# Kernel optimization log

Measured on AMD Instinct MI355X. Metric: run time of the kernel, lower is better.

Reference implementation:

```python
import math
import jax, jax.numpy as jnp
import numpy as np
from jax.scipy.special import xlogy

B, N, INP, E = 128, 16, 1024, 512
MU, CLF, PLCY = 512, 512, 512
M = N - 1          # merges (full tree)
T = N + M          # total tree tokens
L = N + M - 1      # logits matrix side
NOISE_STD, MASK_VAL = 0.01, -9e20
SFTMX_EPS, STD_EPS = 1e-20, 1e-20


def _mlp3(x, w1, b1, w2, b2, w3, b3):
    h = jax.nn.relu(x @ w1 + b1)
    h = jax.nn.relu(h @ w2 + b2)
    return h @ w3 + b3


def _lin(key, fi, fo):
    lim = math.sqrt(6.0 / (fi + fo))  # xavier uniform
    return (jax.random.uniform(key, (fi, fo), minval=-lim, maxval=lim, dtype=jnp.float32),
            jnp.full((fo,), 0.001, dtype=jnp.float32))


def setup_inputs():
    key = jax.random.key(0)
    ks = jax.random.split(key, 16)
    inp = {"x": jax.random.normal(ks[0], (B, N, INP), dtype=jnp.float32)}
    inp["lift_w"], inp["lift_b"] = _lin(ks[1], INP, E)
    inp["unlift_w"], inp["unlift_b"] = _lin(ks[2], E, INP)
    inp["enc_w1"], inp["enc_b1"] = _lin(ks[3], 2 * E, MU)
    inp["enc_w2"], inp["enc_b2"] = _lin(ks[4], MU, MU)
    inp["enc_w3"], inp["enc_b3"] = _lin(ks[5], MU, E)
    inp["dec_w1"], inp["dec_b1"] = _lin(ks[6], E, MU)
    inp["dec_w2"], inp["dec_b2"] = _lin(ks[7], MU, MU)
    inp["dec_w3"], inp["dec_b3"] = _lin(ks[8], MU, 2 * E)
    inp["clf_w1"], inp["clf_b1"] = _lin(ks[9], E, CLF)
    inp["clf_w2"], inp["clf_b2"] = _lin(ks[10], CLF, CLF)
    inp["clf_w3"], inp["clf_b3"] = _lin(ks[11], CLF, 2)
    inp["pol_w1"], inp["pol_b1"] = _lin(ks[12], 2 * E, PLCY)
    inp["pol_w2"], inp["pol_b2"] = _lin(ks[13], PLCY, PLCY)
    inp["pol_w3"], inp["pol_b3"] = _lin(ks[14], PLCY, 1)
    return inp


def _forward(x, lift_w, lift_b, unlift_w, unlift_b,
             enc_w1, enc_b1, enc_w2, enc_b2, enc_w3, enc_b3,
             dec_w1, dec_b1, dec_w2, dec_b2, dec_w3, dec_b3,
             clf_w1, clf_b1, clf_w2, clf_b2, clf_w3, clf_b3,
             pol_w1, pol_b1, pol_w2, pol_b2, pol_w3, pol_b3):
    sg = jax.lax.stop_gradient
    enc = lambda z: _mlp3(z, enc_w1, enc_b1, enc_w2, enc_b2, enc_w3, enc_b3)
    dec = lambda z: _mlp3(z, dec_w1, dec_b1, dec_w2, dec_b2, dec_w3, dec_b3)
    clf = lambda z: _mlp3(z, clf_w1, clf_b1, clf_w2, clf_b2, clf_w3, clf_b3)
    pol = lambda z: _mlp3(z, pol_w1, pol_b1, pol_w2, pol_b2, pol_w3, pol_b3)
    base = jax.random.key(42)
    b_idx = jnp.arange(B)

    # lift + noise
    u = x @ lift_w + lift_b
    u = u + NOISE_STD * jax.random.normal(jax.random.fold_in(base, 7), u.shape, u.dtype)

    logits_mtx = jnp.full((B, L, L), MASK_VAL, dtype=jnp.float32)
    # iter 0: score all ordered pairs (i,j), i != j, among input tokens (vectorized)
    ii, jj = np.where(~np.eye(N, dtype=bool))                 # P = N*(N-1) static pairs
    pair_x = jnp.concatenate([u[:, ii], u[:, jj]], axis=-1)   # [B,P,2E]
    logits_mtx = logits_mtx.at[:, ii, jj].set(pol(sg(pair_x))[..., 0])

    active = jnp.tile(jnp.arange(N, dtype=jnp.int32), (B, 1))
    step_losses = jnp.zeros(B, dtype=jnp.float32)
    entropies = jnp.zeros(B, dtype=jnp.float32)
    actions, log_probs, rewards = [], [], []

    for it in range(M):
        A = active.shape[1]  # = N - it (active-token count at entry)
        if it > 0:
            nt = N + it - 1                      # newest merged token (last in active)
            act = active[:, :-1]                 # [B, A-1] older active tokens
            u_act = u[b_idx[:, None], act]       # [B, A-1, E]
            u_nt = jnp.broadcast_to(u[:, nt][:, None, :], u_act.shape)
            lg_f = pol(sg(jnp.concatenate([u_nt, u_act], -1)))[..., 0]
            lg_b = pol(sg(jnp.concatenate([u_act, u_nt], -1)))[..., 0]
            logits_mtx = logits_mtx.at[b_idx[:, None], nt, act].set(lg_f)
            logits_mtx = logits_mtx.at[b_idx[:, None], act, nt].set(lg_b)

        flat = logits_mtx.reshape(B, L * L)      # temp == 1 for learned policy
        p = jax.nn.softmax(flat, axis=1)
        P2 = L * L
        p_adj = (p + SFTMX_EPS) / (1.0 + P2 * SFTMX_EPS)
        val_norm = SFTMX_EPS / (1.0 + P2 * SFTMX_EPS)
        opt_norm = A * (A - 1)
        nopt = P2 - opt_norm
        entrop = -(jnp.sum(xlogy(p_adj, p_adj), axis=1)
                   - nopt * (val_norm * math.log(val_norm))) / math.log(opt_norm)
        entropies = entropies + entrop

        # multinomial sample over flattened (masked) logits matrix
        sflat = jax.random.categorical(jax.random.fold_in(base, 100 + it), flat)
        s0, s1 = sflat // L, sflat % L
        sample = jnp.stack([s0, s1], axis=1)     # [B,2]
        actions.append(sample)
        log_probs.append(jnp.log(p[b_idx, sflat]))

        # mask out rows/cols of the merged tokens
        logits_mtx = logits_mtx.at[b_idx[:, None], sample, :].set(MASK_VAL)
        logits_mtx = logits_mtx.at[b_idx[:, None], :, sample].set(MASK_VAL)

        # remove the two sampled tokens from the active set (order-preserving)
        keep = (active != s0[:, None].astype(active.dtype)) & (active != s1[:, None].astype(active.dtype))
        order = jnp.argsort((~keep).astype(jnp.int32), axis=1, stable=True)
        active = jnp.take_along_axis(active, order[:, :A - 2], axis=1)

        pair = jnp.concatenate([u[b_idx, s0], u[b_idx, s1]], axis=1)  # [B,2E]
        true_s = sg(pair)
        pred_s = dec(enc(true_s))
        osl = jnp.sum((pred_s - true_s) ** 2, axis=1) / (2 * E)
        step_losses = step_losses + osl
        rewards.append(-sg(osl))

        # merge: encode pair (grad flows into u here) + noise, append to tree
        mg = enc(pair)
        mg = mg + NOISE_STD * jax.random.normal(jax.random.fold_in(base, 1000 + it), mg.shape, mg.dtype)
        u = jnp.concatenate([u, mg[:, None, :]], axis=1)
        active = jnp.concatenate([active, jnp.full((B, 1), N + it, dtype=active.dtype)], axis=1)

    actions = jnp.stack(actions, axis=1)    # [B,M,2]
    log_probs = jnp.stack(log_probs, axis=1)
    rewards = jnp.stack(rewards, axis=1)

    # top-down decode
    d = jnp.zeros_like(u)
    d = d.at[b_idx[:, None], active].set(u[b_idx[:, None], active])  # seed remaining active (root)
    clf_rows = []
    for it in range(M):
        tok = T - 1 - it
        mgd = d[:, tok]
        unmg = dec(mgd).reshape(B, 2, E)
        d = d.at[b_idx[:, None], actions[:, M - 1 - it]].set(unmg)
        clf_rows.append(clf(sg(mgd)))
    clf_pred = jnp.concatenate(
        [jnp.stack(clf_rows, axis=1), clf(sg(d[:, :N]))[:, ::-1, :]], axis=1)  # [B,M+N,2]
    clf_lbl = jnp.tile(jnp.concatenate(
        [jnp.ones(M, dtype=jnp.int32), jnp.zeros(N, dtype=jnp.int32)]), (B, 1))

    step_losses = step_losses / M
    entropies = entropies / M
    mvg = rewards.reshape(-1)  # B*M <= mvg_adv_sz, so moving buffer == current rewards
    rew_n = (rewards - mvg.mean()) / (jnp.std(mvg, ddof=1) + STD_EPS)
    reinf = jnp.sum(log_probs * rew_n, axis=1)
    recon = d[:, :N] @ unlift_w + unlift_b
    return recon, u, d, step_losses, entropies, clf_pred, clf_lbl, reinf


def reference(x, lift_w, lift_b, unlift_w, unlift_b,
              enc_w1, enc_b1, enc_w2, enc_b2, enc_w3, enc_b3,
              dec_w1, dec_b1, dec_w2, dec_b2, dec_w3, dec_b3,
              clf_w1, clf_b1, clf_w2, clf_b2, clf_w3, clf_b3,
              pol_w1, pol_b1, pol_w2, pol_b2, pol_w3, pol_b3):
    return _forward(x, lift_w, lift_b, unlift_w, unlift_b,
                    enc_w1, enc_b1, enc_w2, enc_b2, enc_w3, enc_b3,
                    dec_w1, dec_b1, dec_w2, dec_b2, dec_w3, dec_b3,
                    clf_w1, clf_b1, clf_w2, clf_b2, clf_w3, clf_b3,
                    pol_w1, pol_b1, pol_w2, pol_b2, pol_w3, pol_b3)
```

## Files before the change

kernel.cpp:

```cpp
#include <hip/hip_runtime.h>
#include <cstdint>
#include <cmath>

#define MASKV -9.0e20f

__host__ __device__ inline void tf2x32(uint32_t k0, uint32_t k1, uint32_t& x0, uint32_t& x1){
  uint32_t ks2 = k0 ^ k1 ^ 0x1BD11BDAu;
  x0 += k0; x1 += k1;
#define TFR(r) { x0 += x1; x1 = (x1<<(r))|(x1>>(32-(r))); x1 ^= x0; }
  TFR(13) TFR(15) TFR(26) TFR(6)
  x0 += k1;  x1 += ks2 + 1u;
  TFR(17) TFR(29) TFR(16) TFR(24)
  x0 += ks2; x1 += k0 + 2u;
  TFR(13) TFR(15) TFR(26) TFR(6)
  x0 += k0;  x1 += k1 + 3u;
  TFR(17) TFR(29) TFR(16) TFR(24)
  x0 += k1;  x1 += ks2 + 4u;
  TFR(13) TFR(15) TFR(26) TFR(6)
  x0 += ks2; x1 += k0 + 5u;
#undef TFR
}

__device__ inline uint32_t rbits32(uint32_t k0, uint32_t k1, uint32_t idx){
  uint32_t x0 = 0u, x1 = idx;
  tf2x32(k0, k1, x0, x1);
  return x0 ^ x1;
}

__device__ inline float u01_from_bits(uint32_t bits){
  union { uint32_t u; float f; } c;
  c.u = (bits >> 9) | 0x3f800000u;
  return c.f - 1.0f;
}

__device__ inline float erfinv_f(float x){
  float w = -log1pf(-x*x);
  float p;
  if (w < 5.0f){
    w -= 2.5f;
    p = 2.81022636e-08f;
    p = fmaf(p, w, 3.43273939e-07f);
    p = fmaf(p, w, -3.5233877e-06f);
    p = fmaf(p, w, -4.39150654e-06f);
    p = fmaf(p, w, 0.00021858087f);
    p = fmaf(p, w, -0.00125372503f);
    p = fmaf(p, w, -0.00417768164f);
    p = fmaf(p, w, 0.246640727f);
    p = fmaf(p, w, 1.50140941f);
  } else {
    w = sqrtf(w) - 3.0f;
    p = -0.000200214257f;
    p = fmaf(p, w, 0.000100950558f);
    p = fmaf(p, w, 0.00134934322f);
    p = fmaf(p, w, -0.00367342844f);
    p = fmaf(p, w, 0.00573950773f);
    p = fmaf(p, w, -0.0076224613f);
    p = fmaf(p, w, 0.00943887047f);
    p = fmaf(p, w, 1.00167406f);
    p = fmaf(p, w, 2.83297682f);
  }
  return p * x;
}

__device__ inline float jax_normal(uint32_t k0, uint32_t k1, uint32_t idx){
  float f = u01_from_bits(rbits32(k0, k1, idx));
  float v = fmaf(f, 2.0f, -0.99999994f);
  v = fmaxf(v, -0.99999994f);
  return 1.41421356f * erfinv_f(v);
}

__device__ inline float jax_gumbel(uint32_t k0, uint32_t k1, uint32_t idx){
  float f = u01_from_bits(rbits32(k0, k1, idx));
  f = f + 1.17549435e-38f;
  f = fmaxf(f, 1.17549435e-38f);
  return -logf(-logf(f));
}

template<int ACT>
__global__ __launch_bounds__(256) void gemm_k(
    const float* __restrict__ A, int lda,
    const long* __restrict__ atab, int anblk,
    const float* __restrict__ W, const float* __restrict__ bias,
    float* __restrict__ C, int K, int N,
    long c_base, int c_rdiv, long c_ostride, long c_istride)
{
  __shared__ float As[16][64];
  __shared__ float Ws[16][64];
  int tid = threadIdx.x;
  int c0 = blockIdx.x * 64;
  int r0 = blockIdx.y * 64;
  int lr = tid >> 2;
  int lk = (tid & 3) << 2;
  int wk = tid >> 4;
  int wc = (tid & 15) << 2;
  int tx = tid & 15;
  int ty = tid >> 4;
  long aoff0 = 0, aoff1 = 0;
  if (atab){
    const long* t = atab + (long)(r0 + lr) * anblk;
    aoff0 = t[0];
    if (anblk == 2) aoff1 = t[1];
  } else {
    aoff0 = (long)(r0 + lr) * lda;
  }
  float acc[4][4];
#pragma unroll
  for (int i = 0; i < 4; i++)
#pragma unroll
    for (int j = 0; j < 4; j++) acc[i][j] = 0.f;

  for (int k0 = 0; k0 < K; k0 += 16){
    int ka = k0 + lk;
    long ab = (atab && anblk == 2 && ka >= 512) ? (aoff1 + (ka - 512)) : (aoff0 + ka);
    float4 av = *(const float4*)(A + ab);
    As[lk + 0][lr] = av.x;
    As[lk + 1][lr] = av.y;
    As[lk + 2][lr] = av.z;
    As[lk + 3][lr] = av.w;
    float4 wv = *(const float4*)(W + (long)(k0 + wk) * N + (c0 + wc));
    *(float4*)&Ws[wk][wc] = wv;
    __syncthreads();
#pragma unroll
    for (int kk = 0; kk < 16; kk++){
      float4 a4 = *(const float4*)&As[kk][ty << 2];
      float4 w4 = *(const float4*)&Ws[kk][tx << 2];
      float aa[4] = {a4.x, a4.y, a4.z, a4.w};
      float ww[4] = {w4.x, w4.y, w4.z, w4.w};
#pragma unroll
      for (int i = 0; i < 4; i++)
#pragma unroll
        for (int j = 0; j < 4; j++)
          acc[i][j] = fmaf(aa[i], ww[j], acc[i][j]);
    }
    __syncthreads();
  }
  float4 bv = *(const float4*)(bias + c0 + (tx << 2));
  float bb[4] = {bv.x, bv.y, bv.z, bv.w};
#pragma unroll
  for (int i = 0; i < 4; i++){
    int r = r0 + (ty << 2) + i;
    long off = c_base + (long)(r / c_rdiv) * c_ostride + (long)(r % c_rdiv) * c_istride
               + c0 + (tx << 2);
    float4 v;
    float o0 = acc[i][0] + bb[0], o1 = acc[i][1] + bb[1];
    float o2 = acc[i][2] + bb[2], o3 = acc[i][3] + bb[3];
    if (ACT){ o0 = fmaxf(o0, 0.f); o1 = fmaxf(o1, 0.f); o2 = fmaxf(o2, 0.f); o3 = fmaxf(o3, 0.f); }
    v.x = o0; v.y = o1; v.z = o2; v.w = o3;
    *(float4*)(C + off) = v;
  }
}

__global__ __launch_bounds__(512, 7) void gemm128f_k(
    const float* __restrict__ Y,
    const long* __restrict__ atab,
    const float* __restrict__ b1,
    const float* __restrict__ W2, const float* __restrict__ b2,
    const float* __restrict__ w3,
    const int* __restrict__ scat, float* __restrict__ logits)
{
  __shared__ float As[16][132];
  __shared__ float Ws[16][132];
  int tid = threadIdx.x;
  int c0 = blockIdx.x * 128;
  int r0 = blockIdx.y * 128;
  int tx = tid & 15, ty = tid >> 4;
  int rA = tid >> 2;
  int kq = (tid & 3) << 2;
  long a0r = atab[(long)(r0 + rA) * 2];
  long a1r = atab[(long)(r0 + rA) * 2 + 1];
  int wk = tid >> 5;
  int wc = (tid & 31) << 2;
  float acc[4][8];
#pragma unroll
  for (int i = 0; i < 4; i++)
#pragma unroll
    for (int j = 0; j < 8; j++) acc[i][j] = 0.f;

  for (int k0 = 0; k0 < 512; k0 += 16){
    int ka = k0 + kq;
    float4 p = *(const float4*)(Y + a0r + ka);
    float4 q = *(const float4*)(Y + a1r + ka);
    float4 bb = *(const float4*)(b1 + ka);
    As[kq + 0][rA] = fmaxf(p.x + q.x + bb.x, 0.f);
    As[kq + 1][rA] = fmaxf(p.y + q.y + bb.y, 0.f);
    As[kq + 2][rA] = fmaxf(p.z + q.z + bb.z, 0.f);
    As[kq + 3][rA] = fmaxf(p.w + q.w + bb.w, 0.f);
    *(float4*)&Ws[wk][wc] = *(const float4*)(W2 + (long)(k0 + wk) * 512 + (c0 + wc));
    __syncthreads();
#pragma unroll
    for (int kk = 0; kk < 16; kk++){
      float a4[4], w8[8];
      *(float4*)&a4[0] = *(const float4*)&As[kk][ty << 2];
      *(float4*)&w8[0] = *(const float4*)&Ws[kk][tx << 2];
      *(float4*)&w8[4] = *(const float4*)&Ws[kk][(tx << 2) + 64];
#pragma unroll
      for (int i = 0; i < 4; i++)
#pragma unroll
        for (int j = 0; j < 8; j++)
          acc[i][j] = fmaf(a4[i], w8[j], acc[i][j]);
    }
    __syncthreads();
  }
  float bb[8], w3v[8];
  *(float4*)&bb[0]  = *(const float4*)(b2 + c0 + (tx << 2));
  *(float4*)&bb[4]  = *(const float4*)(b2 + c0 + (tx << 2) + 64);
  *(float4*)&w3v[0] = *(const float4*)(w3 + c0 + (tx << 2));
  *(float4*)&w3v[4] = *(const float4*)(w3 + c0 + (tx << 2) + 64);
#pragma unroll
  for (int i = 0; i < 4; i++){
    float p = 0.f;
#pragma unroll
    for (int j = 0; j < 8; j++)
      p = fmaf(fmaxf(acc[i][j] + bb[j], 0.f), w3v[j], p);
    for (int m = 1; m < 16; m <<= 1) p += __shfl_xor(p, m);
    if (tx == 0){
      int rr = (ty << 2) + i;
      atomicAdd(logits + scat[r0 + rr], p);
    }
  }
}

__global__ __launch_bounds__(256) void gemm64f_k(
    const float* __restrict__ Y,
    const long* __restrict__ atab,
    const float* __restrict__ b1,
    const float* __restrict__ W2, const float* __restrict__ b2,
    const float* __restrict__ w3,
    const int* __restrict__ scat, float* __restrict__ logits)
{
  __shared__ float As[16][64];
  __shared__ float Ws[16][64];
  int tid = threadIdx.x;
  int c0 = blockIdx.x * 64;
  int r0 = blockIdx.y * 64;
  int lr = tid >> 2;
  int lk = (tid & 3) << 2;
  int wk = tid >> 4;
  int wc = (tid & 15) << 2;
  int tx = tid & 15;
  int ty = tid >> 4;
  long a0 = atab[(long)(r0 + lr) * 2];
  long a1 = atab[(long)(r0 + lr) * 2 + 1];
  float acc[4][4];
#pragma unroll
  for (int i = 0; i < 4; i++)
#pragma unroll
    for (int j = 0; j < 4; j++) acc[i][j] = 0.f;

  for (int k0 = 0; k0 < 512; k0 += 16){
    int ka = k0 + lk;
    float4 p = *(const float4*)(Y + a0 + ka);
    float4 q = *(const float4*)(Y + a1 + ka);
    float4 bb = *(const float4*)(b1 + ka);
    As[lk + 0][lr] = fmaxf(p.x + q.x + bb.x, 0.f);
    As[lk + 1][lr] = fmaxf(p.y + q.y + bb.y, 0.f);
    As[lk + 2][lr] = fmaxf(p.z + q.z + bb.z, 0.f);
    As[lk + 3][lr] = fmaxf(p.w + q.w + bb.w, 0.f);
    *(float4*)&Ws[wk][wc] = *(const float4*)(W2 + (long)(k0 + wk) * 512 + (c0 + wc));
    __syncthreads();
#pragma unroll
    for (int kk = 0; kk < 16; kk++){
      float4 a4 = *(const float4*)&As[kk][ty << 2];
      float4 w4 = *(const float4*)&Ws[kk][tx << 2];
      float aa[4] = {a4.x, a4.y, a4.z, a4.w};
      float ww[4] = {w4.x, w4.y, w4.z, w4.w};
#pragma unroll
      for (int i = 0; i < 4; i++)
#pragma unroll
        for (int j = 0; j < 4; j++)
          acc[i][j] = fmaf(aa[i], ww[j], acc[i][j]);
    }
    __syncthreads();
  }
  float bb4[4], w34[4];
  *(float4*)&bb4[0] = *(const float4*)(b2 + c0 + (tx << 2));
  *(float4*)&w34[0] = *(const float4*)(w3 + c0 + (tx << 2));
#pragma unroll
  for (int i = 0; i < 4; i++){
    float p = 0.f;
#pragma unroll
    for (int j = 0; j < 4; j++)
      p = fmaf(fmaxf(acc[i][j] + bb4[j], 0.f), w34[j], p);
    for (int m = 1; m < 16; m <<= 1) p += __shfl_xor(p, m);
    if (tx == 0){
      int r = r0 + (ty << 2) + i;
      atomicAdd(logits + scat[r], p);
    }
  }
}

__global__ __launch_bounds__(256) void rowdot2_k(
    const float* __restrict__ A, int lda,
    const float* __restrict__ W, const float* __restrict__ bias,
    int K, float* __restrict__ out, const int* __restrict__ scat)
{
  int wid = threadIdx.x >> 6, lane = threadIdx.x & 63;
  int r = blockIdx.x * 4 + wid;
  const float* a = A + (long)r * lda;
  float s0 = 0.f, s1 = 0.f;
  for (int k = lane; k < K; k += 64){
    float x = a[k];
    s0 = fmaf(x, W[k * 2], s0);
    s1 = fmaf(x, W[k * 2 + 1], s1);
  }
  for (int off = 32; off > 0; off >>= 1){
    s0 += __shfl_down(s0, off);
    s1 += __shfl_down(s1, off);
  }
  if (lane == 0){
    long o = scat[r];
    out[o] = s0 + bias[0];
    out[o + 1] = s1 + bias[1];
  }
}

__global__ __launch_bounds__(256) void pairmv_k(
    const float* __restrict__ u, const long* __restrict__ tab_pair,
    const float* __restrict__ W, const float* __restrict__ bias,
    float* __restrict__ dst)
{
  __shared__ float s[1024];
  int b = blockIdx.y, tid = threadIdx.x;
  int c = blockIdx.x * 256 + tid;
  long t0 = tab_pair[b * 2], t1 = tab_pair[b * 2 + 1];
  s[tid]       = u[t0 + tid];
  s[tid + 256] = u[t0 + tid + 256];
  s[tid + 512] = u[t1 + tid];
  s[tid + 768] = u[t1 + tid + 256];
  __syncthreads();
  float a0 = 0.f, a1 = 0.f, a2 = 0.f, a3 = 0.f;
#pragma unroll 8
  for (int k = 0; k < 1024; k += 4){
    a0 = fmaf(s[k],     W[(long)k * 512 + c],       a0);
    a1 = fmaf(s[k + 1], W[(long)(k + 1) * 512 + c], a1);
    a2 = fmaf(s[k + 2], W[(long)(k + 2) * 512 + c], a2);
    a3 = fmaf(s[k + 3], W[(long)(k + 3) * 512 + c], a3);
  }
  float v = ((a0 + a1) + (a2 + a3)) + bias[c];
  dst[(long)b * 512 + c] = fmaxf(v, 0.f);
}

__global__ __launch_bounds__(256) void mvrelu_k(
    const float* __restrict__ src, long sstride,
    const float* __restrict__ W, const float* __restrict__ bias,
    float* __restrict__ dst)
{
  __shared__ float s[512];
  int b = blockIdx.y, tid = threadIdx.x;
  int c = blockIdx.x * 256 + tid;
  const float* sr = src + (long)b * sstride;
  s[tid] = sr[tid];
  s[tid + 256] = sr[tid + 256];
  __syncthreads();
  float a0 = 0.f, a1 = 0.f, a2 = 0.f, a3 = 0.f;
#pragma unroll 8
  for (int k = 0; k < 512; k += 4){
    a0 = fmaf(s[k],     W[(long)k * 512 + c],       a0);
    a1 = fmaf(s[k + 1], W[(long)(k + 1) * 512 + c], a1);
    a2 = fmaf(s[k + 2], W[(long)(k + 2) * 512 + c], a2);
    a3 = fmaf(s[k + 3], W[(long)(k + 3) * 512 + c], a3);
  }
  float v = ((a0 + a1) + (a2 + a3)) + bias[c];
  dst[(long)b * 512 + c] = fmaxf(v, 0.f);
}

__global__ __launch_bounds__(256) void lay3z_k(
    const float* __restrict__ src,
    const float* __restrict__ W, const float* __restrict__ bias,
    float* __restrict__ z_all, float* __restrict__ u,
    int it, uint32_t k0, uint32_t k1)
{
  __shared__ float s[512];
  int b = blockIdx.y, tid = threadIdx.x;
  int c = blockIdx.x * 256 + tid;
  const float* sr = src + (long)b * 512;
  s[tid] = sr[tid];
  s[tid + 256] = sr[tid + 256];
  __syncthreads();
  float a0 = 0.f, a1 = 0.f, a2 = 0.f, a3 = 0.f;
#pragma unroll 8
  for (int k = 0; k < 512; k += 4){
    a0 = fmaf(s[k],     W[(long)k * 512 + c],       a0);
    a1 = fmaf(s[k + 1], W[(long)(k + 1) * 512 + c], a1);
    a2 = fmaf(s[k + 2], W[(long)(k + 2) * 512 + c], a2);
    a3 = fmaf(s[k + 3], W[(long)(k + 3) * 512 + c], a3);
  }
  float v = ((a0 + a1) + (a2 + a3)) + bias[c];
  z_all[(long)it * 65536 + (long)b * 512 + c] = v;
  float nv = jax_normal(k0, k1, (uint32_t)(b * 512 + c));
  u[((long)(b * 31 + 16 + it)) * 512 + c] = v + 0.01f * nv;
}

__global__ __launch_bounds__(256) void yrow_k(
    const float* __restrict__ u, const float* __restrict__ W1cat,
    float* __restrict__ Y, int it)
{
  __shared__ float s[512];
  int b = blockIdx.y, tid = threadIdx.x;
  int c = blockIdx.x * 256 + tid;
  const float* sr = u + ((long)(b * 31 + 16 + it)) * 512;
  s[tid] = sr[tid];
  s[tid + 256] = sr[tid + 256];
  __syncthreads();
  float a0 = 0.f, a1 = 0.f, a2 = 0.f, a3 = 0.f;
#pragma unroll 8
  for (int k = 0; k < 512; k += 4){
    a0 = fmaf(s[k],     W1cat[(long)k * 1024 + c],       a0);
    a1 = fmaf(s[k + 1], W1cat[(long)(k + 1) * 1024 + c], a1);
    a2 = fmaf(s[k + 2], W1cat[(long)(k + 2) * 1024 + c], a2);
    a3 = fmaf(s[k + 3], W1cat[(long)(k + 3) * 1024 + c], a3);
  }
  Y[((long)(b * 31 + 16 + it)) * 1024 + c] = (a0 + a1) + (a2 + a3);
}

__global__ __launch_bounds__(256) void rev3_k(
    const float* __restrict__ src,
    const float* __restrict__ W, const float* __restrict__ bias,
    float* __restrict__ dmat, const int* __restrict__ actions, int it)
{
  __shared__ float s[512];
  int b = blockIdx.y, tid = threadIdx.x;
  int p = blockIdx.x * 256 + tid;
  const float* sr = src + (long)b * 512;
  s[tid] = sr[tid];
  s[tid + 256] = sr[tid + 256];
  __syncthreads();
  float a0 = 0.f, a1 = 0.f, a2 = 0.f, a3 = 0.f;
#pragma unroll 8
  for (int k = 0; k < 512; k += 4){
    a0 = fmaf(s[k],     W[(long)k * 1024 + p],       a0);
    a1 = fmaf(s[k + 1], W[(long)(k + 1) * 1024 + p], a1);
    a2 = fmaf(s[k + 2], W[(long)(k + 2) * 1024 + p], a2);
    a3 = fmaf(s[k + 3], W[(long)(k + 3) * 1024 + p], a3);
  }
  float v = ((a0 + a1) + (a2 + a3)) + bias[p];
  int fit = 14 - it;
  int s0 = actions[(b * 15 + fit) * 2];
  int s1 = actions[(b * 15 + fit) * 2 + 1];
  int node = (p < 512) ? s0 : s1;
  int ee = p & 511;
  dmat[((long)(b * 31 + node)) * 512 + ee] = v;
}

__global__ __launch_bounds__(256) void oslb_k(
    const float* __restrict__ pred, const float* __restrict__ u,
    const int* __restrict__ actions, float* __restrict__ sl, float* __restrict__ rew)
{
  int r = blockIdx.x, tid = threadIdx.x;
  int it = r >> 7, b = r & 127;
  int s0 = actions[(b * 15 + it) * 2];
  int s1 = actions[(b * 15 + it) * 2 + 1];
  const float* t0 = u + ((long)(b * 31 + s0)) * 512;
  const float* t1 = u + ((long)(b * 31 + s1)) * 512;
  const float* p = pred + (long)r * 1024;
  float s = 0.f;
  for (int k = tid; k < 512; k += 256){
    float d0 = p[k] - t0[k];       s = fmaf(d0, d0, s);
    float d1 = p[k + 512] - t1[k]; s = fmaf(d1, d1, s);
  }
  __shared__ float red[256];
  red[tid] = s; __syncthreads();
  for (int st = 128; st > 0; st >>= 1){ if (tid < st) red[tid] += red[tid + st]; __syncthreads(); }
  if (tid == 0){
    float osl = red[0] / 1024.0f;
    atomicAdd(sl + b, osl);
    rew[b * 15 + it] = -osl;
  }
}

__global__ __launch_bounds__(256) void init_k(float* __restrict__ lbl,
    float* __restrict__ logits, float* __restrict__ sl, float* __restrict__ ent,
    int* __restrict__ active, float* __restrict__ zb,
    float* __restrict__ W1cat, const float* __restrict__ pol_w1, const float* __restrict__ pol_b3,
    long* __restrict__ tab_init, int* __restrict__ scat_init, long* __restrict__ tab_tok16,
    long* __restrict__ tab_mgd, int* __restrict__ scat_clf, long clf_off)
{
  long i = (long)blockIdx.x * 256 + threadIdx.x;
  if (i < 524288L){
    int k = (int)(i >> 10), n = (int)(i & 1023);
    W1cat[i] = (n < 512) ? pol_w1[(long)k * 512 + n] : pol_w1[(long)(k + 512) * 512 + (n - 512)];
  }
  if (i < 115200L){
    int rem = (int)(i % 900);
    int rr = rem / 30, cc = rem % 30;
    logits[i] = (rr < 16 && cc < 16 && rr != cc) ? pol_b3[0] : MASKV;
  }
  if (i < 30720L){
    int r = (int)i;
    int pk = r >> 7, b = r & 127;
    int ii2 = pk / 15, jr = pk % 15;
    int jj2 = jr + (jr >= ii2 ? 1 : 0);
    tab_init[r * 2]     = ((long)(b * 31 + ii2)) * 1024;
    tab_init[r * 2 + 1] = ((long)(b * 31 + jj2)) * 1024 + 512;
    scat_init[r] = b * 900 + ii2 * 30 + jj2;
  }
  if (i < 3968L){
    lbl[i] = ((i % 31) < 15) ? 1.0f : 0.0f;
    int r = (int)i;
    if (r < 1920){
      scat_clf[r] = (int)(clf_off + (long)(r & 127) * 62 + (r >> 7) * 2);
    } else {
      int rr = r - 1920;
      scat_clf[r] = (int)(clf_off + (long)(rr >> 4) * 62 + 60 - ((rr & 15) << 1));
    }
  }
  if (i < 2048L){
    active[i] = (int)(i & 15);
    tab_tok16[i] = ((long)((i >> 4) * 31 + (i & 15))) * 512;
  }
  if (i < 1920L){
    int it = (int)(i >> 7), b = (int)(i & 127);
    tab_mgd[i] = ((long)(b * 31 + 30 - it)) * 512;
  }
  if (i < 1024L)  zb[i] = 0.f;
  if (i < 128L){ sl[i] = 0.f; ent[i] = 0.f; }
}

__global__ __launch_bounds__(256) void noise_u_k(float* __restrict__ u, uint32_t k0, uint32_t k1){
  uint32_t e = blockIdx.x * 256u + threadIdx.x;
  uint32_t b = e >> 13, rem = e & 8191u, n = rem >> 9, ee = rem & 511u;
  float nr = jax_normal(k0, k1, e);
  long off = ((long)(b * 31u + n)) * 512 + ee;
  u[off] += 0.01f * nr;
}

__global__ __launch_bounds__(256) void build_d_k(float* __restrict__ dmat, const float* __restrict__ u){
  int e = blockIdx.x * 256 + threadIdx.x;
  int b = e >> 9, ee = e & 511;
  long off = ((long)(b * 31 + 30)) * 512 + ee;
  dmat[off] = u[off];
}

__global__ __launch_bounds__(256) void sample_k(float* __restrict__ logits, int* __restrict__ active,
    int* __restrict__ actions, float* __restrict__ lp, float* __restrict__ ent,
    int it, int A, uint32_t k0, uint32_t k1, float log_opt,
    long* __restrict__ tab_loop, int* __restrict__ scat_loop, long* __restrict__ tab_pair,
    const float* __restrict__ pol_b3)
{
  int b = blockIdx.x, tid = threadIdx.x;
  int lane = tid & 63, wid = tid >> 6;
  float* Lg = logits + (long)b * 900;
  __shared__ float rmax[4], rS[4], rT[4], rG[4];
  __shared__ int rGi[4];
  __shared__ int ss0, ss1;

  float v = -3.4e38f;
  for (int j = tid; j < 900; j += 256) v = fmaxf(v, Lg[j]);
#pragma unroll
  for (int m = 32; m; m >>= 1) v = fmaxf(v, __shfl_xor(v, m));
  if (lane == 0) rmax[wid] = v;
  __syncthreads();
  float mx = fmaxf(fmaxf(rmax[0], rmax[1]), fmaxf(rmax[2], rmax[3]));

  float s = 0.f, t = 0.f;
  for (int j = tid; j < 900; j += 256){
    float l = Lg[j];
    float d = l - mx;
    float e = expf(d);
    s += e;
    if (l > MASKV) t = fmaf(e, d, t);
  }
#pragma unroll
  for (int m = 32; m; m >>= 1){ s += __shfl_xor(s, m); t += __shfl_xor(t, m); }
  if (lane == 0){ rS[wid] = s; rT[wid] = t; }

  float bv = -3.4e38f; int bi = 0;
  for (int j = tid; j < 900; j += 256){
    float g = jax_gumbel(k0, k1, (uint32_t)(b * 900 + j));
    float val = Lg[j] + g;
    if (val > bv){ bv = val; bi = j; }
  }
#pragma unroll
  for (int m = 32; m; m >>= 1){
    float ov = __shfl_xor(bv, m); int oi = __shfl_xor(bi, m);
    if (ov > bv || (ov == bv && oi < bi)){ bv = ov; bi = oi; }
  }
  if (lane == 0){ rG[wid] = bv; rGi[wid] = bi; }
  __syncthreads();

  if (tid == 0){
    float S = (rS[0] + rS[1]) + (rS[2] + rS[3]);
    float T = (rT[0] + rT[1]) + (rT[2] + rT[3]);
    ent[b] += -(T / S - logf(S)) / log_opt;
    float gb = rG[0]; int gi = rGi[0];
    for (int w = 1; w < 4; w++){
      if (rG[w] > gb || (rG[w] == gb && rGi[w] < gi)){ gb = rG[w]; gi = rGi[w]; }
    }
    int sf = gi;
    int s0 = sf / 30, s1 = sf % 30;
    ss0 = s0; ss1 = s1;
    actions[(b * 15 + it) * 2] = s0;
    actions[(b * 15 + it) * 2 + 1] = s1;
    lp[b * 15 + it] = Lg[sf] - mx - logf(S);
    tab_pair[b * 2]     = ((long)(b * 31 + s0)) * 512;
    tab_pair[b * 2 + 1] = ((long)(b * 31 + s1)) * 512;
  }
  __syncthreads();
  int s0 = ss0, s1 = ss1;
  if (tid < 30){
    Lg[s0 * 30 + tid] = MASKV;
    Lg[s1 * 30 + tid] = MASKV;
    Lg[tid * 30 + s0] = MASKV;
    Lg[tid * 30 + s1] = MASKV;
  }
  if (tid == 0){
    float b3v = pol_b3[0];
    int buf[16]; int c = 0;
    for (int k = 0; k < A; k++){
      int a = active[b * 16 + k];
      if (a != s0 && a != s1) buf[c++] = a;
    }
    int nt2 = 16 + it;
    buf[c++] = nt2;
    for (int k = 0; k < c; k++) active[b * 16 + k] = buf[k];
    int na2 = c - 1;
    for (int j = 0; j < na2; j++){
      int q = buf[j];
      int r1 = j * 128 + b;
      tab_loop[r1 * 2]     = ((long)(b * 31 + nt2)) * 1024;
      tab_loop[r1 * 2 + 1] = ((long)(b * 31 + q)) * 1024 + 512;
      int sc1 = b * 900 + nt2 * 30 + q;
      scat_loop[r1] = sc1;
      logits[sc1] = b3v;
      int r2 = (na2 + j) * 128 + b;
      tab_loop[r2 * 2]     = ((long)(b * 31 + q)) * 1024;
      tab_loop[r2 * 2 + 1] = ((long)(b * 31 + nt2)) * 1024 + 512;
      int sc2 = b * 900 + q * 30 + nt2;
      scat_loop[r2] = sc2;
      logits[sc2] = b3v;
    }
  }
}

__global__ __launch_bounds__(256) void finalize_k(const float* __restrict__ rew,
    const float* __restrict__ lp, const float* __restrict__ sl, const float* __restrict__ ent,
    float* __restrict__ out_sl, float* __restrict__ out_ent, float* __restrict__ out_reinf)
{
  __shared__ float red[256];
  int tid = threadIdx.x;
  float s = 0.f;
  for (int i = tid; i < 1920; i += 256) s += rew[i];
  red[tid] = s; __syncthreads();
  for (int st = 128; st > 0; st >>= 1){ if (tid < st) red[tid] += red[tid + st]; __syncthreads(); }
  float mean = red[0] / 1920.0f; __syncthreads();
  float v = 0.f;
  for (int i = tid; i < 1920; i += 256){ float x = rew[i] - mean; v = fmaf(x, x, v); }
  red[tid] = v; __syncthreads();
  for (int st = 128; st > 0; st >>= 1){ if (tid < st) red[tid] += red[tid + st]; __syncthreads(); }
  float denom = sqrtf(red[0] / 1919.0f) + 1e-20f;
  if (tid < 128){
    out_sl[tid] = sl[tid] / 15.0f;
    out_ent[tid] = ent[tid] / 15.0f;
    float r = 0.f;
    for (int k = 0; k < 15; k++){
      float rn = (rew[tid * 15 + k] - mean) / denom;
      r = fmaf(lp[tid * 15 + k], rn, r);
    }
    out_reinf[tid] = r;
  }
}

extern "C" void kernel_launch(void* const* d_in, const int* in_sizes, int n_in,
                              void* d_out, int out_size, void* d_ws, size_t ws_size,
                              hipStream_t stream)
{
  const float* x        = (const float*)d_in[0];
  const float* lift_w   = (const float*)d_in[1];
  const float* lift_b   = (const float*)d_in[2];
  const float* unlift_w = (const float*)d_in[3];
  const float* unlift_b = (const float*)d_in[4];
  const float* enc_w1   = (const float*)d_in[5];
  const float* enc_b1   = (const float*)d_in[6];
  const float* enc_w2   = (const float*)d_in[7];
  const float* enc_b2   = (const float*)d_in[8];
  const float* enc_w3   = (const float*)d_in[9];
  const float* enc_b3   = (const float*)d_in[10];
  const float* dec_w1   = (const float*)d_in[11];
  const float* dec_b1   = (const float*)d_in[12];
  const float* dec_w2   = (const float*)d_in[13];
  const float* dec_b2   = (const float*)d_in[14];
  const float* dec_w3   = (const float*)d_in[15];
  const float* dec_b3   = (const float*)d_in[16];
  const float* clf_w1   = (const float*)d_in[17];
  const float* clf_b1   = (const float*)d_in[18];
  const float* clf_w2   = (const float*)d_in[19];
  const float* clf_b2   = (const float*)d_in[20];
  const float* clf_w3   = (const float*)d_in[21];
  const float* clf_b3   = (const float*)d_in[22];
  const float* pol_w1   = (const float*)d_in[23];
  const float* pol_b1   = (const float*)d_in[24];
  const float* pol_w2   = (const float*)d_in[25];
  const float* pol_b2   = (const float*)d_in[26];
  const float* pol_w3   = (const float*)d_in[27];
  const float* pol_b3   = (const float*)d_in[28];

  float* out = (float*)d_out;
  const long U_OFF     = 2097152;
  const long D_OFF     = 4128768;
  const long SL_OFF    = 6160384;
  const long ENT_OFF   = 6160512;
  const long CLF_OFF   = 6160640;
  const long LBL_OFF   = 6168576;
  const long REINF_OFF = 6172544;
  float* recon = out;
  float* u     = out + U_OFF;
  float* dmat  = out + D_OFF;

  char* wsb = (char*)d_ws;
  size_t wo = 0;
  auto alloc = [&](size_t bytes) -> void* {
    void* p = (void*)(wsb + wo);
    wo = (wo + bytes + 255) & ~(size_t)255;
    return p;
  };
  float* logits    = (float*)alloc(115200 * 4);
  float* Y         = (float*)alloc((size_t)3968 * 1024 * 4);
  float* h1clf     = Y;
  float* pbuf      = Y + 2031616;
  float* h2clf     = Y + 2031616;
  float* W1cat     = (float*)alloc((size_t)524288 * 4);
  float* zb        = (float*)alloc(1024 * 4);
  float* h1        = (float*)alloc((size_t)2048 * 512 * 4);
  float* h2        = (float*)alloc((size_t)2048 * 512 * 4);
  float* z_all     = (float*)alloc((size_t)15 * 65536 * 4);
  float* sl        = (float*)alloc(128 * 4);
  float* ent       = (float*)alloc(128 * 4);
  float* lp        = (float*)alloc(1920 * 4);
  float* rew       = (float*)alloc(1920 * 4);
  int*   active    = (int*)alloc(2048 * 4);
  int*   actions   = (int*)alloc(3840 * 4);
  long*  tab_init  = (long*)alloc((size_t)30720 * 2 * 8);
  int*   scat_init = (int*)alloc(30720 * 4);
  long*  tab_loop  = (long*)alloc((size_t)3584 * 2 * 8);
  int*   scat_loop = (int*)alloc(3584 * 4);
  long*  tab_pair  = (long*)alloc(256 * 8);
  long*  tab_mgd   = (long*)alloc(1920 * 8);
  long*  tab_tok16 = (long*)alloc(2048 * 8);
  int*   scat_clf  = (int*)alloc(3968 * 4);
  long*  tab_clf   = tab_mgd;
  (void)ws_size; (void)in_sizes; (void)n_in; (void)out_size;

  uint32_t k7a, k7b, ck0[15], ck1[15], mk0[15], mk1[15];
  { uint32_t a = 0, b = 7; tf2x32(0u, 42u, a, b); k7a = a; k7b = b; }
  for (int it = 0; it < 15; it++){
    { uint32_t a = 0, b = (uint32_t)(100 + it); tf2x32(0u, 42u, a, b); ck0[it] = a; ck1[it] = b; }
    { uint32_t a = 0, b = (uint32_t)(1000 + it); tf2x32(0u, 42u, a, b); mk0[it] = a; mk1[it] = b; }
  }

  auto gemm = [&](int act, const float* A, int lda, const long* atab, int anblk,
                  const float* W, const float* bs, float* C, int rows, int K, int Nn,
                  long cb, int crd, long cos, long cis){
    dim3 g(Nn / 64, rows / 64);
    if (act) gemm_k<1><<<g, 256, 0, stream>>>(A, lda, atab, anblk, W, bs, C, K, Nn, cb, crd, cos, cis);
    else     gemm_k<0><<<g, 256, 0, stream>>>(A, lda, atab, anblk, W, bs, C, K, Nn, cb, crd, cos, cis);
  };

  init_k<<<2048, 256, 0, stream>>>(out + LBL_OFF, logits, sl, ent, active, zb,
                                   W1cat, pol_w1, pol_b3, tab_init, scat_init, tab_tok16,
                                   tab_mgd, scat_clf, CLF_OFF);

  gemm(0, x, 1024, nullptr, 0, lift_w, lift_b, u, 2048, 1024, 512, 0, 16, 15872, 512);
  noise_u_k<<<4096, 256, 0, stream>>>(u, k7a, k7b);

  gemm(0, u, 0, tab_tok16, 1, W1cat, zb, Y, 2048, 512, 1024, 0, 16, 31744, 1024);

  { dim3 g(4, 240);
    gemm128f_k<<<g, 512, 0, stream>>>(Y, tab_init, pol_b1, pol_w2, pol_b2, pol_w3,
                                      scat_init, logits); }

  for (int it = 0; it < 15; it++){
    int A = 16 - it;
    if (it > 0){
      int rows = 256 * (15 - it);
      dim3 g(8, rows / 64);
      gemm64f_k<<<g, 256, 0, stream>>>(Y, tab_loop, pol_b1, pol_w2, pol_b2, pol_w3,
                                       scat_loop, logits);
    }
    float log_opt = (float)log((double)(A * (A - 1)));
    sample_k<<<128, 256, 0, stream>>>(logits, active, actions, lp, ent, it, A,
                                      ck0[it], ck1[it], log_opt,
                                      tab_loop, scat_loop, tab_pair, pol_b3);
    { dim3 g(2, 128);
      pairmv_k<<<g, 256, 0, stream>>>(u, tab_pair, enc_w1, enc_b1, h1); }
    { dim3 g(2, 128);
      mvrelu_k<<<g, 256, 0, stream>>>(h1, 512, enc_w2, enc_b2, h2); }
    { dim3 g(2, 128);
      lay3z_k<<<g, 256, 0, stream>>>(h2, enc_w3, enc_b3, z_all, u, it, mk0[it], mk1[it]); }
    if (it < 14){
      dim3 g(4, 128);
      yrow_k<<<g, 256, 0, stream>>>(u, W1cat, Y, it);
    }
  }

  gemm(1, z_all, 512, nullptr, 0, dec_w1, dec_b1, h1, 1920, 512, 512, 0, 1, 512, 0);
  gemm(1, h1, 512, nullptr, 0, dec_w2, dec_b2, h2, 1920, 512, 512, 0, 1, 512, 0);
  gemm(0, h2, 512, nullptr, 0, dec_w3, dec_b3, pbuf, 1920, 512, 1024, 0, 1, 1024, 0);
  oslb_k<<<1920, 256, 0, stream>>>(pbuf, u, actions, sl, rew);

  build_d_k<<<256, 256, 0, stream>>>(dmat, u);

  for (int it = 0; it < 15; it++){
    int tok = 30 - it;
    { dim3 g(2, 128);
      mvrelu_k<<<g, 256, 0, stream>>>(dmat + (long)tok * 512, 15872, dec_w1, dec_b1, h1); }
    { dim3 g(2, 128);
      mvrelu_k<<<g, 256, 0, stream>>>(h1, 512, dec_w2, dec_b2, h2); }
    { dim3 g(4, 128);
      rev3_k<<<g, 256, 0, stream>>>(h2, dec_w3, dec_b3, dmat, actions, it); }
  }

  gemm(1, dmat, 0, tab_clf, 1, clf_w1, clf_b1, h1clf, 3968, 512, 512, 0, 1, 512, 0);
  gemm(1, h1clf, 512, nullptr, 0, clf_w2, clf_b2, h2clf, 3968, 512, 512, 0, 1, 512, 0);
  rowdot2_k<<<992, 256, 0, stream>>>(h2clf, 512, clf_w3, clf_b3, 512, out, scat_clf);

  gemm(0, dmat, 0, tab_tok16, 1, unlift_w, unlift_b, recon, 2048, 512, 1024,
       0, 16, 16384, 1024);

  finalize_k<<<1, 256, 0, stream>>>(rew, lp, sl, ent,
                                    out + SL_OFF, out + ENT_OFF, out + REINF_OFF);
}
```

Baseline: 2.568 ms.

## Batch four rows per block in sequential matvec kernels and enlarge policy GEMM tile

The per-step matrix-vector kernels in the encoder and decoder loops now handle four batch rows per block, so each weight element loaded from global memory feeds four rows instead of one. This cuts weight traffic per step fourfold but launches a quarter as many blocks. The initial fused policy GEMM now uses a 256-row tile with an 8x8 register tile per thread and a lower occupancy hint, giving more reuse per block at the cost of fewer blocks and more register pressure.

```diff
diff --git a/kernel.cpp b/kernel.cpp
--- a/kernel.cpp
+++ b/kernel.cpp
@@ -150,7 +150,7 @@
   }
 }
 
-__global__ __launch_bounds__(512, 7) void gemm128f_k(
+__global__ __launch_bounds__(512, 4) void gemm128f_k(
     const float* __restrict__ Y,
     const long* __restrict__ atab,
     const float* __restrict__ b1,
@@ -158,46 +158,53 @@
     const float* __restrict__ w3,
     const int* __restrict__ scat, float* __restrict__ logits)
 {
-  __shared__ float As[16][132];
+  __shared__ float As[16][260];
   __shared__ float Ws[16][132];
   int tid = threadIdx.x;
   int c0 = blockIdx.x * 128;
-  int r0 = blockIdx.y * 128;
+  int r0 = blockIdx.y * 256;
   int tx = tid & 15, ty = tid >> 4;
-  int rA = tid >> 2;
-  int kq = (tid & 3) << 2;
+  int rA = tid >> 1;
+  int kh = (tid & 1) << 3;
   long a0r = atab[(long)(r0 + rA) * 2];
   long a1r = atab[(long)(r0 + rA) * 2 + 1];
   int wk = tid >> 5;
   int wc = (tid & 31) << 2;
-  float acc[4][8];
-#pragma unroll
-  for (int i = 0; i < 4; i++)
+  float acc[8][8];
+#pragma unroll
+  for (int i = 0; i < 8; i++)
 #pragma unroll
     for (int j = 0; j < 8; j++) acc[i][j] = 0.f;
 
   for (int k0 = 0; k0 < 512; k0 += 16){
-    int ka = k0 + kq;
-    float4 p = *(const float4*)(Y + a0r + ka);
-    float4 q = *(const float4*)(Y + a1r + ka);
-    float4 bb = *(const float4*)(b1 + ka);
-    As[kq + 0][rA] = fmaxf(p.x + q.x + bb.x, 0.f);
-    As[kq + 1][rA] = fmaxf(p.y + q.y + bb.y, 0.f);
-    As[kq + 2][rA] = fmaxf(p.z + q.z + bb.z, 0.f);
-    As[kq + 3][rA] = fmaxf(p.w + q.w + bb.w, 0.f);
+    float4 p0 = *(const float4*)(Y + a0r + k0 + kh);
+    float4 p1 = *(const float4*)(Y + a0r + k0 + kh + 4);
+    float4 q0 = *(const float4*)(Y + a1r + k0 + kh);
+    float4 q1 = *(const float4*)(Y + a1r + k0 + kh + 4);
+    float4 bv0 = *(const float4*)(b1 + k0 + kh);
+    float4 bv1 = *(const float4*)(b1 + k0 + kh + 4);
+    As[kh + 0][rA] = fmaxf(p0.x + q0.x + bv0.x, 0.f);
+    As[kh + 1][rA] = fmaxf(p0.y + q0.y + bv0.y, 0.f);
+    As[kh + 2][rA] = fmaxf(p0.z + q0.z + bv0.z, 0.f);
+    As[kh + 3][rA] = fmaxf(p0.w + q0.w + bv0.w, 0.f);
+    As[kh + 4][rA] = fmaxf(p1.x + q1.x + bv1.x, 0.f);
+    As[kh + 5][rA] = fmaxf(p1.y + q1.y + bv1.y, 0.f);
+    As[kh + 6][rA] = fmaxf(p1.z + q1.z + bv1.z, 0.f);
+    As[kh + 7][rA] = fmaxf(p1.w + q1.w + bv1.w, 0.f);
     *(float4*)&Ws[wk][wc] = *(const float4*)(W2 + (long)(k0 + wk) * 512 + (c0 + wc));
     __syncthreads();
 #pragma unroll
     for (int kk = 0; kk < 16; kk++){
-      float a4[4], w8[8];
-      *(float4*)&a4[0] = *(const float4*)&As[kk][ty << 2];
+      float a8[8], w8[8];
+      *(float4*)&a8[0] = *(const float4*)&As[kk][ty << 3];
+      *(float4*)&a8[4] = *(const float4*)&As[kk][(ty << 3) + 4];
       *(float4*)&w8[0] = *(const float4*)&Ws[kk][tx << 2];
       *(float4*)&w8[4] = *(const float4*)&Ws[kk][(tx << 2) + 64];
 #pragma unroll
-      for (int i = 0; i < 4; i++)
+      for (int i = 0; i < 8; i++)
 #pragma unroll
         for (int j = 0; j < 8; j++)
-          acc[i][j] = fmaf(a4[i], w8[j], acc[i][j]);
+          acc[i][j] = fmaf(a8[i], w8[j], acc[i][j]);
     }
     __syncthreads();
   }
@@ -207,14 +214,14 @@
   *(float4*)&w3v[0] = *(const float4*)(w3 + c0 + (tx << 2));
   *(float4*)&w3v[4] = *(const float4*)(w3 + c0 + (tx << 2) + 64);
 #pragma unroll
-  for (int i = 0; i < 4; i++){
+  for (int i = 0; i < 8; i++){
     float p = 0.f;
 #pragma unroll
     for (int j = 0; j < 8; j++)
       p = fmaf(fmaxf(acc[i][j] + bb[j], 0.f), w3v[j], p);
     for (int m = 1; m < 16; m <<= 1) p += __shfl_xor(p, m);
     if (tx == 0){
-      int rr = (ty << 2) + i;
+      int rr = (ty << 3) + i;
       atomicAdd(logits + scat[r0 + rr], p);
     }
   }
@@ -314,132 +321,171 @@
   }
 }
 
-__global__ __launch_bounds__(256) void pairmv_k(
-    const float* __restrict__ u, const long* __restrict__ tab_pair,
+template<int ACT>
+__global__ __launch_bounds__(256) void bmv4_k(
+    const float* __restrict__ src, long sbase, long sstride,
+    const long* __restrict__ tab,
     const float* __restrict__ W, const float* __restrict__ bias,
-    float* __restrict__ dst)
-{
-  __shared__ float s[1024];
-  int b = blockIdx.y, tid = threadIdx.x;
+    int K, int N, float* __restrict__ dst, long dbase, long dstride)
+{
+  __shared__ float s[4][1024];
+  int tid = threadIdx.x;
+  int lane = tid & 63, wid = tid >> 6;
+  int b0 = blockIdx.y * 4;
   int c = blockIdx.x * 256 + tid;
-  long t0 = tab_pair[b * 2], t1 = tab_pair[b * 2 + 1];
-  s[tid]       = u[t0 + tid];
-  s[tid + 256] = u[t0 + tid + 256];
-  s[tid + 512] = u[t1 + tid];
-  s[tid + 768] = u[t1 + tid + 256];
+  if (tab){
+    long t0 = tab[(long)(b0 + wid) * 2];
+    long t1 = tab[(long)(b0 + wid) * 2 + 1];
+    if (lane < 32){
+      int k0 = lane << 4;
+      *(float4*)&s[wid][k0]      = *(const float4*)(src + t0 + k0);
+      *(float4*)&s[wid][k0 + 4]  = *(const float4*)(src + t0 + k0 + 4);
+      *(float4*)&s[wid][k0 + 8]  = *(const float4*)(src + t0 + k0 + 8);
+      *(float4*)&s[wid][k0 + 12] = *(const float4*)(src + t0 + k0 + 12);
+    } else {
+      int k0 = (lane - 32) << 4;
+      *(float4*)&s[wid][512 + k0]      = *(const float4*)(src + t1 + k0);
+      *(float4*)&s[wid][512 + k0 + 4]  = *(const float4*)(src + t1 + k0 + 4);
+      *(float4*)&s[wid][512 + k0 + 8]  = *(const float4*)(src + t1 + k0 + 8);
+      *(float4*)&s[wid][512 + k0 + 12] = *(const float4*)(src + t1 + k0 + 12);
+    }
+  } else {
+    const float* sr = src + sbase + (long)(b0 + wid) * sstride;
+    int k0 = lane << 3;
+    *(float4*)&s[wid][k0]     = *(const float4*)(sr + k0);
+    *(float4*)&s[wid][k0 + 4] = *(const float4*)(sr + k0 + 4);
+  }
   __syncthreads();
-  float a0 = 0.f, a1 = 0.f, a2 = 0.f, a3 = 0.f;
-#pragma unroll 8
-  for (int k = 0; k < 1024; k += 4){
-    a0 = fmaf(s[k],     W[(long)k * 512 + c],       a0);
-    a1 = fmaf(s[k + 1], W[(long)(k + 1) * 512 + c], a1);
-    a2 = fmaf(s[k + 2], W[(long)(k + 2) * 512 + c], a2);
-    a3 = fmaf(s[k + 3], W[(long)(k + 3) * 512 + c], a3);
-  }
-  float v = ((a0 + a1) + (a2 + a3)) + bias[c];
-  dst[(long)b * 512 + c] = fmaxf(v, 0.f);
-}
-
-__global__ __launch_bounds__(256) void mvrelu_k(
-    const float* __restrict__ src, long sstride,
-    const float* __restrict__ W, const float* __restrict__ bias,
-    float* __restrict__ dst)
-{
-  __shared__ float s[512];
-  int b = blockIdx.y, tid = threadIdx.x;
-  int c = blockIdx.x * 256 + tid;
-  const float* sr = src + (long)b * sstride;
-  s[tid] = sr[tid];
-  s[tid + 256] = sr[tid + 256];
-  __syncthreads();
-  float a0 = 0.f, a1 = 0.f, a2 = 0.f, a3 = 0.f;
-#pragma unroll 8
-  for (int k = 0; k < 512; k += 4){
-    a0 = fmaf(s[k],     W[(long)k * 512 + c],       a0);
-    a1 = fmaf(s[k + 1], W[(long)(k + 1) * 512 + c], a1);
-    a2 = fmaf(s[k + 2], W[(long)(k + 2) * 512 + c], a2);
-    a3 = fmaf(s[k + 3], W[(long)(k + 3) * 512 + c], a3);
-  }
-  float v = ((a0 + a1) + (a2 + a3)) + bias[c];
-  dst[(long)b * 512 + c] = fmaxf(v, 0.f);
-}
-
-__global__ __launch_bounds__(256) void lay3z_k(
+  float acc[4][4];
+#pragma unroll
+  for (int bi = 0; bi < 4; bi++)
+#pragma unroll
+    for (int j = 0; j < 4; j++) acc[bi][j] = 0.f;
+
+#pragma unroll 4
+  for (int k = 0; k < K; k += 4){
+    float wv0 = W[(long)k * N + c];
+    float wv1 = W[(long)(k + 1) * N + c];
+    float wv2 = W[(long)(k + 2) * N + c];
+    float wv3 = W[(long)(k + 3) * N + c];
+#pragma unroll
+    for (int bi = 0; bi < 4; bi++){
+      float4 sv = *(const float4*)&s[bi][k];
+      acc[bi][0] = fmaf(sv.x, wv0, acc[bi][0]);
+      acc[bi][1] = fmaf(sv.y, wv1, acc[bi][1]);
+      acc[bi][2] = fmaf(sv.z, wv2, acc[bi][2]);
+      acc[bi][3] = fmaf(sv.w, wv3, acc[bi][3]);
+    }
+  }
+  float bc = bias[c];
+#pragma unroll
+  for (int bi = 0; bi < 4; bi++){
+    float v = ((acc[bi][0] + acc[bi][1]) + (acc[bi][2] + acc[bi][3])) + bc;
+    if (ACT) v = fmaxf(v, 0.f);
+    dst[dbase + (long)(b0 + bi) * dstride + c] = v;
+  }
+}
+
+__global__ __launch_bounds__(256) void lay3z4_k(
     const float* __restrict__ src,
     const float* __restrict__ W, const float* __restrict__ bias,
     float* __restrict__ z_all, float* __restrict__ u,
     int it, uint32_t k0, uint32_t k1)
 {
-  __shared__ float s[512];
-  int b = blockIdx.y, tid = threadIdx.x;
+  __shared__ float s[4][512];
+  int tid = threadIdx.x;
+  int lane = tid & 63, wid = tid >> 6;
+  int b0 = blockIdx.y * 4;
   int c = blockIdx.x * 256 + tid;
-  const float* sr = src + (long)b * 512;
-  s[tid] = sr[tid];
-  s[tid + 256] = sr[tid + 256];
+  {
+    const float* sr = src + (long)(b0 + wid) * 512;
+    int kk = lane << 3;
+    *(float4*)&s[wid][kk]     = *(const float4*)(sr + kk);
+    *(float4*)&s[wid][kk + 4] = *(const float4*)(sr + kk + 4);
+  }
   __syncthreads();
-  float a0 = 0.f, a1 = 0.f, a2 = 0.f, a3 = 0.f;
-#pragma unroll 8
+  float acc[4][4];
+#pragma unroll
+  for (int bi = 0; bi < 4; bi++)
+#pragma unroll
+    for (int j = 0; j < 4; j++) acc[bi][j] = 0.f;
+
+#pragma unroll 4
   for (int k = 0; k < 512; k += 4){
-    a0 = fmaf(s[k],     W[(long)k * 512 + c],       a0);
-    a1 = fmaf(s[k + 1], W[(long)(k + 1) * 512 + c], a1);
-    a2 = fmaf(s[k + 2], W[(long)(k + 2) * 512 + c], a2);
-    a3 = fmaf(s[k + 3], W[(long)(k + 3) * 512 + c], a3);
-  }
-  float v = ((a0 + a1) + (a2 + a3)) + bias[c];
-  z_all[(long)it * 65536 + (long)b * 512 + c] = v;
-  float nv = jax_normal(k0, k1, (uint32_t)(b * 512 + c));
-  u[((long)(b * 31 + 16 + it)) * 512 + c] = v + 0.01f * nv;
-}
-
-__global__ __launch_bounds__(256) void yrow_k(
-    const float* __restrict__ u, const float* __restrict__ W1cat,
-    float* __restrict__ Y, int it)
-{
-  __shared__ float s[512];
-  int b = blockIdx.y, tid = threadIdx.x;
-  int c = blockIdx.x * 256 + tid;
-  const float* sr = u + ((long)(b * 31 + 16 + it)) * 512;
-  s[tid] = sr[tid];
-  s[tid + 256] = sr[tid + 256];
-  __syncthreads();
-  float a0 = 0.f, a1 = 0.f, a2 = 0.f, a3 = 0.f;
-#pragma unroll 8
-  for (int k = 0; k < 512; k += 4){
-    a0 = fmaf(s[k],     W1cat[(long)k * 1024 + c],       a0);
-    a1 = fmaf(s[k + 1], W1cat[(long)(k + 1) * 1024 + c], a1);
-    a2 = fmaf(s[k + 2], W1cat[(long)(k + 2) * 1024 + c], a2);
-    a3 = fmaf(s[k + 3], W1cat[(long)(k + 3) * 1024 + c], a3);
-  }
-  Y[((long)(b * 31 + 16 + it)) * 1024 + c] = (a0 + a1) + (a2 + a3);
-}
-
-__global__ __launch_bounds__(256) void rev3_k(
+    float wv0 = W[(long)k * 512 + c];
+    float wv1 = W[(long)(k + 1) * 512 + c];
+    float wv2 = W[(long)(k + 2) * 512 + c];
+    float wv3 = W[(long)(k + 3) * 512 + c];
+#pragma unroll
+    for (int bi = 0; bi < 4; bi++){
+      float4 sv = *(const float4*)&s[bi][k];
+      acc[bi][0] = fmaf(sv.x, wv0, acc[bi][0]);
+      acc[bi][1] = fmaf(sv.y, wv1, acc[bi][1]);
+      acc[bi][2] = fmaf(sv.z, wv2, acc[bi][2]);
+      acc[bi][3] = fmaf(sv.w, wv3, acc[bi][3]);
+    }
+  }
+  float bc = bias[c];
+#pragma unroll
+  for (int bi = 0; bi < 4; bi++){
+    int b = b0 + bi;
+    float v = ((acc[bi][0] + acc[bi][1]) + (acc[bi][2] + acc[bi][3])) + bc;
+    z_all[(long)it * 65536 + (long)b * 512 + c] = v;
+    float nv = jax_normal(k0, k1, (uint32_t)(b * 512 + c));
+    u[((long)(b * 31 + 16 + it)) * 512 + c] = v + 0.01f * nv;
+  }
+}
+
+__global__ __launch_bounds__(256) void rev34_k(
     const float* __restrict__ src,
     const float* __restrict__ W, const float* __restrict__ bias,
     float* __restrict__ dmat, const int* __restrict__ actions, int it)
 {
-  __shared__ float s[512];
-  int b = blockIdx.y, tid = threadIdx.x;
+  __shared__ float s[4][512];
+  int tid = threadIdx.x;
+  int lane = tid & 63, wid = tid >> 6;
+  int b0 = blockIdx.y * 4;
   int p = blockIdx.x * 256 + tid;
-  const float* sr = src + (long)b * 512;
-  s[tid] = sr[tid];
-  s[tid + 256] = sr[tid + 256];
+  {
+    const float* sr = src + (long)(b0 + wid) * 512;
+    int kk = lane << 3;
+    *(float4*)&s[wid][kk]     = *(const float4*)(sr + kk);
+    *(float4*)&s[wid][kk + 4] = *(const float4*)(sr + kk + 4);
+  }
   __syncthreads();
-  float a0 = 0.f, a1 = 0.f, a2 = 0.f, a3 = 0.f;
-#pragma unroll 8
+  float acc[4][4];
+#pragma unroll
+  for (int bi = 0; bi < 4; bi++)
+#pragma unroll
+    for (int j = 0; j < 4; j++) acc[bi][j] = 0.f;
+
+#pragma unroll 4
   for (int k = 0; k < 512; k += 4){
-    a0 = fmaf(s[k],     W[(long)k * 1024 + p],       a0);
-    a1 = fmaf(s[k + 1], W[(long)(k + 1) * 1024 + p], a1);
-    a2 = fmaf(s[k + 2], W[(long)(k + 2) * 1024 + p], a2);
-    a3 = fmaf(s[k + 3], W[(long)(k + 3) * 1024 + p], a3);
-  }
-  float v = ((a0 + a1) + (a2 + a3)) + bias[p];
+    float wv0 = W[(long)k * 1024 + p];
+    float wv1 = W[(long)(k + 1) * 1024 + p];
+    float wv2 = W[(long)(k + 2) * 1024 + p];
+    float wv3 = W[(long)(k + 3) * 1024 + p];
+#pragma unroll
+    for (int bi = 0; bi < 4; bi++){
+      float4 sv = *(const float4*)&s[bi][k];
+      acc[bi][0] = fmaf(sv.x, wv0, acc[bi][0]);
+      acc[bi][1] = fmaf(sv.y, wv1, acc[bi][1]);
+      acc[bi][2] = fmaf(sv.z, wv2, acc[bi][2]);
+      acc[bi][3] = fmaf(sv.w, wv3, acc[bi][3]);
+    }
+  }
+  float bc = bias[p];
   int fit = 14 - it;
-  int s0 = actions[(b * 15 + fit) * 2];
-  int s1 = actions[(b * 15 + fit) * 2 + 1];
-  int node = (p < 512) ? s0 : s1;
   int ee = p & 511;
-  dmat[((long)(b * 31 + node)) * 512 + ee] = v;
+#pragma unroll
+  for (int bi = 0; bi < 4; bi++){
+    int b = b0 + bi;
+    float v = ((acc[bi][0] + acc[bi][1]) + (acc[bi][2] + acc[bi][3])) + bc;
+    int s0 = actions[(b * 15 + fit) * 2];
+    int s1 = actions[(b * 15 + fit) * 2 + 1];
+    int node = (p < 512) ? s0 : s1;
+    dmat[((long)(b * 31 + node)) * 512 + ee] = v;
+  }
 }
 
 __global__ __launch_bounds__(256) void oslb_k(
@@ -764,7 +810,7 @@
 
   gemm(0, u, 0, tab_tok16, 1, W1cat, zb, Y, 2048, 512, 1024, 0, 16, 31744, 1024);
 
-  { dim3 g(4, 240);
+  { dim3 g(4, 120);
     gemm128f_k<<<g, 512, 0, stream>>>(Y, tab_init, pol_b1, pol_w2, pol_b2, pol_w3,
                                       scat_init, logits); }
 
@@ -780,15 +826,18 @@
     sample_k<<<128, 256, 0, stream>>>(logits, active, actions, lp, ent, it, A,
                                       ck0[it], ck1[it], log_opt,
                                       tab_loop, scat_loop, tab_pair, pol_b3);
-    { dim3 g(2, 128);
-      pairmv_k<<<g, 256, 0, stream>>>(u, tab_pair, enc_w1, enc_b1, h1); }
-    { dim3 g(2, 128);
-      mvrelu_k<<<g, 256, 0, stream>>>(h1, 512, enc_w2, enc_b2, h2); }
-    { dim3 g(2, 128);
-      lay3z_k<<<g, 256, 0, stream>>>(h2, enc_w3, enc_b3, z_all, u, it, mk0[it], mk1[it]); }
+    { dim3 g(2, 32);
+      bmv4_k<1><<<g, 256, 0, stream>>>(u, 0, 0, tab_pair, enc_w1, enc_b1,
+                                       1024, 512, h1, 0, 512); }
+    { dim3 g(2, 32);
+      bmv4_k<1><<<g, 256, 0, stream>>>(h1, 0, 512, nullptr, enc_w2, enc_b2,
+                                       512, 512, h2, 0, 512); }
+    { dim3 g(2, 32);
+      lay3z4_k<<<g, 256, 0, stream>>>(h2, enc_w3, enc_b3, z_all, u, it, mk0[it], mk1[it]); }
     if (it < 14){
-      dim3 g(4, 128);
-      yrow_k<<<g, 256, 0, stream>>>(u, W1cat, Y, it);
+      dim3 g(4, 32);
+      bmv4_k<0><<<g, 256, 0, stream>>>(u, (long)(16 + it) * 512, 15872, nullptr, W1cat, zb,
+                                       512, 1024, Y, (long)(16 + it) * 1024, 31744);
     }
   }
 
@@ -801,12 +850,14 @@
 
   for (int it = 0; it < 15; it++){
     int tok = 30 - it;
-    { dim3 g(2, 128);
-      mvrelu_k<<<g, 256, 0, stream>>>(dmat + (long)tok * 512, 15872, dec_w1, dec_b1, h1); }
-    { dim3 g(2, 128);
-      mvrelu_k<<<g, 256, 0, stream>>>(h1, 512, dec_w2, dec_b2, h2); }
-    { dim3 g(4, 128);
-      rev3_k<<<g, 256, 0, stream>>>(h2, dec_w3, dec_b3, dmat, actions, it); }
+    { dim3 g(2, 32);
+      bmv4_k<1><<<g, 256, 0, stream>>>(dmat, (long)tok * 512, 15872, nullptr, dec_w1, dec_b1,
+                                       512, 512, h1, 0, 512); }
+    { dim3 g(2, 32);
+      bmv4_k<1><<<g, 256, 0, stream>>>(h1, 0, 512, nullptr, dec_w2, dec_b2,
+                                       512, 512, h2, 0, 512); }
+    { dim3 g(4, 32);
+      rev34_k<<<g, 256, 0, stream>>>(h2, dec_w3, dec_b3, dmat, actions, it); }
   }
 
   gemm(1, dmat, 0, tab_clf, 1, clf_w1, clf_b1, h1clf, 3968, 512, 512, 0, 1, 512, 0);
```

Result: slower. 5.125 ms (+99.6%).
